# Optimization experiments

Measured on AMD Instinct MI355X. Metric: run time of the kernel, lower is better.

## Reference

```python
import jax, jax.numpy as jnp
import numpy as np

NEG_INF = -1e10
LEAK = 0.01


def gatconv(x, adj, w, a_param):
    # x: [B, Cin, N]; w: [Cin, Cout]; a_param: [2*Cout, N]; adj: [N, N]
    C = w.shape[1]
    wh = jnp.einsum('biv,io->bov', x, w)                # [B, Cout, N]
    wh1 = jnp.einsum('biv,io->bov', wh, a_param[:C])    # [B, N, N]
    wh2 = jnp.einsum('biv,io->bov', wh, a_param[C:])    # [B, N, N]
    e = jax.nn.leaky_relu(wh1 + wh2, negative_slope=LEAK)
    att = jnp.where(adj[None] > 1e-6, e, NEG_INF)
    att = jax.nn.softmax(att, axis=1)                   # softmax over source nodes (dim 1)
    h = jnp.einsum('bin,bov->bon', att, wh)             # [B, Cout, N]
    return jax.nn.elu(h)                                # GATConv concat=True -> elu


def gat_mh(x, adj, w1, a1, w2, a2):
    # head=1, support_len=1; dropout is identity in eval mode.
    h = jax.nn.elu(gatconv(x, adj, w1, a1))   # inner GAT wrapper elu
    h = jax.nn.elu(gatconv(h, adj, w2, a2))   # out_att GAT wrapper elu
    return jax.nn.elu(h)                      # GAT_MH final elu


def setup_inputs() -> dict:
    key = jax.random.key(0)
    ks = jax.random.split(key, 10)
    B, C, N, T = 8, 32, 512, 12
    inp = jax.random.normal(ks[0], (B, C, N, T), dtype=jnp.float32)
    cell = jax.random.normal(ks[1], (B, C, N, 1), dtype=jnp.float32)
    u = jax.random.uniform(ks[2], (N, N), dtype=jnp.float32)
    adj = jnp.maximum(jnp.where(u < 0.06, 1.0, 0.0), jnp.eye(N, dtype=jnp.float32))
    # 12 timesteps x 8 GAT_MH modules, each = 2 GATConvs (inner head + out_att)
    w1 = jax.random.normal(ks[3], (T, 8, C, C), dtype=jnp.float32) * 0.05
    a1 = jax.random.normal(ks[4], (T, 8, 2 * C, N), dtype=jnp.float32) * 0.05
    w2 = jax.random.normal(ks[5], (T, 8, C, C), dtype=jnp.float32) * 0.05
    a2 = jax.random.normal(ks[6], (T, 8, 2 * C, N), dtype=jnp.float32) * 0.05
    # i/f/o/c biases, each [C, N, T]
    bias = (jax.random.uniform(ks[7], (4, C, N, T), dtype=jnp.float32) - 0.5) * (2.0 / np.sqrt(N))
    return {'input': inp, 'cell': cell, 'adj': adj, 'w1': w1, 'a1': a1, 'w2': w2, 'a2': a2, 'bias': bias}


def reference(input, cell, adj, w1, a1, w2, a2, bias):
    B, C, N, T = input.shape
    c0 = cell[..., 0]                       # [B, C, N]
    xs_t = jnp.moveaxis(input, -1, 0)       # [T, B, C, N]
    bias_t = jnp.moveaxis(bias, -1, 0)      # [T, 4, C, N]

    def step(c, xs):
        x_t, w1t, a1t, w2t, a2t, bt = xs
        stacked = jnp.concatenate([
            jnp.broadcast_to(x_t[None], (4, B, C, N)),
            jnp.broadcast_to(c[None], (4, B, C, N)),
        ], axis=0)                          # [8, B, C, N]
        outs = jax.vmap(gat_mh, in_axes=(0, None, 0, 0, 0, 0))(stacked, adj, w1t, a1t, w2t, a2t)
        g = outs[:4] + bt[:, None]          # gates from x_t, plus per-gate bias
        s = outs[4:]                        # gates from cell
        i = jax.nn.sigmoid(g[0] + s[0])
        f = jax.nn.sigmoid(g[1] + s[1])
        o = jax.nn.sigmoid(g[2] + s[2])
        ct = jnp.tanh(g[3] + s[3])
        c_new = f * c + i * ct
        H = o * jnp.tanh(c_new)
        return c_new, H

    c_final, Hs = jax.lax.scan(step, c0, (xs_t, w1, a1, w2, a2, bias_t))
    output = jnp.moveaxis(Hs, 0, -1)        # [B, C, N, T]
    return output, c_final[..., None]
```

## Files before the change

### kernel.cpp

```cpp
#include <hip/hip_runtime.h>

typedef unsigned long long u64;

#define BB 8
#define CC 32
#define NN 512
#define TT 12
#define NBLK (BB*CC)

__device__ __forceinline__ float eluf(float x) {
  return x > 0.0f ? x : (expf(x) - 1.0f);
}
__device__ __forceinline__ float sigmf(float x) {
  if (x >= 0.0f) return 1.0f / (1.0f + expf(-x));
  float e = expf(x);
  return e / (1.0f + e);
}

__device__ __forceinline__ u64 pack_slot(unsigned tag, float v) {
  return ((u64)tag << 32) | (u64)__float_as_uint(v);
}

__global__ __launch_bounds__(256, 1)
void glstm_fused(const float* __restrict__ xg,
                 const float* __restrict__ cellg,
                 const float* __restrict__ w1g,
                 const float* __restrict__ w2g,
                 const float* __restrict__ biasg,
                 float* __restrict__ outg,
                 u64* slots)
{
  __shared__ float biasL[4][TT][NN];
  __shared__ float preS[4];
  __shared__ float redS[4];
  __shared__ float wpart[13][4];

  const int blk  = blockIdx.x;
  const int b    = blk >> 5;
  const int tid  = threadIdx.x;
  const int lane = tid & 63;
  const int wv   = tid >> 6;
  const int ch   = blk & 31;

  u64* csum_slot = slots;
  u64* xsum_slot = slots + 2*NBLK;

  float c0 = cellg[blk*NN + 2*tid];
  float c1 = cellg[blk*NN + 2*tid + 1];

  float xs[TT];
  #pragma unroll
  for (int t=0;t<TT;t++) xs[t]=0.0f;
  const float* xrow = xg + blk*NN*TT;
  #pragma unroll
  for (int half=0; half<2; half++){
    int n = tid + half*256;
    const float4* p = (const float4*)(xrow + n*TT);
    float4 v0=p[0], v1=p[1], v2=p[2];
    xs[0]+=v0.x;  xs[1]+=v0.y;  xs[2]+=v0.z;  xs[3]+=v0.w;
    xs[4]+=v1.x;  xs[5]+=v1.y;  xs[6]+=v1.z;  xs[7]+=v1.w;
    xs[8]+=v2.x;  xs[9]+=v2.y;  xs[10]+=v2.z; xs[11]+=v2.w;
  }
  float cpart = c0 + c1;
  #pragma unroll
  for (int off=32; off>=1; off>>=1){
    #pragma unroll
    for (int t=0;t<TT;t++) xs[t] += __shfl_xor(xs[t], off, 64);
    cpart += __shfl_xor(cpart, off, 64);
  }
  if (lane == 0){
    #pragma unroll
    for (int t=0;t<TT;t++) wpart[t][wv] = xs[t];
    wpart[12][wv] = cpart;
  }

  #pragma unroll
  for (int k=0;k<4;k++){
    #pragma unroll
    for (int half=0; half<2; half++){
      int n = tid + half*256;
      const float4* p = (const float4*)(biasg + ((k*CC + ch)*NN + n)*TT);
      float4 v0=p[0], v1=p[1], v2=p[2];
      biasL[k][0][n]=v0.x;  biasL[k][1][n]=v0.y;  biasL[k][2][n]=v0.z;  biasL[k][3][n]=v0.w;
      biasL[k][4][n]=v1.x;  biasL[k][5][n]=v1.y;  biasL[k][6][n]=v1.z;  biasL[k][7][n]=v1.w;
      biasL[k][8][n]=v2.x;  biasL[k][9][n]=v2.y;  biasL[k][10][n]=v2.z; biasL[k][11][n]=v2.w;
    }
  }
  __syncthreads();

  if (tid < 13){
    float v = wpart[tid][0] + wpart[tid][1] + wpart[tid][2] + wpart[tid][3];
    u64 pk = pack_slot(1u, v);
    if (tid < TT)
      __hip_atomic_store(&xsum_slot[tid*NBLK + blk], pk,
                         __ATOMIC_RELAXED, __HIP_MEMORY_SCOPE_AGENT);
    else
      __hip_atomic_store(&csum_slot[blk], pk,
                         __ATOMIC_RELAXED, __HIP_MEMORY_SCOPE_AGENT);
  }

  float* outrow = outg + blk*NN*TT;

  for (int s=0; s<TT; s++){
    const int i0 = lane & 31;
    u64* slot = (lane < 32)
      ? &xsum_slot[s*NBLK + b*CC + i0]
      : &csum_slot[(s&1)*NBLK + b*CC + i0];
    const unsigned want = (lane < 32) ? 1u : (unsigned)(s+1);
    u64 v = __hip_atomic_load(slot, __ATOMIC_RELAXED, __HIP_MEMORY_SCOPE_AGENT);
    int guard = 0;
    while ((unsigned)(v >> 32) != want){
      __builtin_amdgcn_s_sleep(1);
      v = __hip_atomic_load(slot, __ATOMIC_RELAXED, __HIP_MEMORY_SCOPE_AGENT);
      if (++guard > 1000000) break;
    }
    float zs = __uint_as_float((unsigned)v);

    const int m = wv + ((lane >> 5) << 2);
    const float* w1m = w1g + (s*8 + m)*CC*CC + i0;
    float s1 = 0.0f;
    #pragma unroll
    for (int j=0;j<CC;j++){
      float a = __shfl(zs, j, 32);
      s1 = fmaf(a, w1m[j*CC], s1);
    }
    float h1 = eluf(eluf(s1));
    float pp = h1 * w2g[((s*8 + m)*CC + i0)*CC + ch];
    #pragma unroll
    for (int off=16; off>=1; off>>=1) pp += __shfl_xor(pp, off, 32);
    float ov = eluf(eluf(eluf(512.0f * pp)));
    float prew = ov + __shfl_xor(ov, 32, 64);
    if (lane == 0) preS[wv] = prew;
    __syncthreads();
    const float g0 = preS[0], g1 = preS[1], g2 = preS[2], g3 = preS[3];

    const int n0 = 2*tid;
    float ig0 = sigmf(g0 + biasL[0][s][n0]);
    float fg0 = sigmf(g1 + biasL[1][s][n0]);
    float ct0 = tanhf(g3 + biasL[3][s][n0]);
    float ig1 = sigmf(g0 + biasL[0][s][n0+1]);
    float fg1 = sigmf(g1 + biasL[1][s][n0+1]);
    float ct1 = tanhf(g3 + biasL[3][s][n0+1]);
    c0 = fg0*c0 + ig0*ct0;
    c1 = fg1*c1 + ig1*ct1;
    float csp = c0 + c1;
    __syncthreads();

    if (s < TT-1){
      #pragma unroll
      for (int off=32; off>=1; off>>=1) csp += __shfl_xor(csp, off, 64);
      if (lane == 0) redS[wv] = csp;
      __syncthreads();
      if (tid == 0){
        float tot = redS[0]+redS[1]+redS[2]+redS[3];
        __hip_atomic_store(&csum_slot[((s+1)&1)*NBLK + blk],
                           pack_slot((unsigned)(s+2), tot),
                           __ATOMIC_RELAXED, __HIP_MEMORY_SCOPE_AGENT);
      }
    }

    float og0 = sigmf(g2 + biasL[2][s][n0]);
    float og1 = sigmf(g2 + biasL[2][s][n0+1]);
    outrow[n0*TT + s]     = og0 * tanhf(c0);
    outrow[(n0+1)*TT + s] = og1 * tanhf(c1);
  }

  float* cf = outg + NBLK*NN*TT + blk*NN;
  cf[2*tid]   = c0;
  cf[2*tid+1] = c1;
}

extern "C" void kernel_launch(void* const* d_in, const int* in_sizes, int n_in,
                              void* d_out, int out_size, void* d_ws, size_t ws_size,
                              hipStream_t stream)
{
  (void)in_sizes; (void)n_in; (void)out_size; (void)ws_size;
  const float* xg    = (const float*)d_in[0];
  const float* cellg = (const float*)d_in[1];
  const float* w1g   = (const float*)d_in[3];
  const float* w2g   = (const float*)d_in[5];
  const float* biasg = (const float*)d_in[7];
  float* outg = (float*)d_out;
  u64* slots = (u64*)d_ws;

  hipMemsetAsync(d_ws, 0, (size_t)(2*NBLK + TT*NBLK)*sizeof(u64), stream);
  glstm_fused<<<dim3(NBLK), dim3(256), 0, stream>>>(xg, cellg, w1g, w2g, biasg, outg, slots);
}
```

Measured before the change: 48.92 us.

## Precompute x-path gates before recurrence and shorten per-step cross-block sync

```diff
diff --git a/kernel.cpp b/kernel.cpp
--- a/kernel.cpp
+++ b/kernel.cpp
@@ -2,26 +2,28 @@
 
 typedef unsigned long long u64;
 
-#define BB 8
 #define CC 32
 #define NN 512
 #define TT 12
-#define NBLK (BB*CC)
-
-__device__ __forceinline__ float eluf(float x) {
-  return x > 0.0f ? x : (expf(x) - 1.0f);
-}
-__device__ __forceinline__ float sigmf(float x) {
-  if (x >= 0.0f) return 1.0f / (1.0f + expf(-x));
-  float e = expf(x);
-  return e / (1.0f + e);
-}
-
-__device__ __forceinline__ u64 pack_slot(unsigned tag, float v) {
-  return ((u64)tag << 32) | (u64)__float_as_uint(v);
-}
-
-__global__ __launch_bounds__(256, 1)
+#define NBLK 256
+#define NTHR 512
+
+__device__ __forceinline__ float eluf(float x){ return x>0.f ? x : (expf(x)-1.f); }
+__device__ __forceinline__ float sigmf(float x){
+  if (x>=0.f) return 1.f/(1.f+expf(-x));
+  float e=expf(x); return e/(1.f+e);
+}
+__device__ __forceinline__ u64 pack_slot(unsigned tag, float v){
+  return ((u64)tag<<32) | (u64)__float_as_uint(v);
+}
+__device__ __forceinline__ u64 ld_slot(u64* p){
+  return __hip_atomic_load(p, __ATOMIC_RELAXED, __HIP_MEMORY_SCOPE_AGENT);
+}
+__device__ __forceinline__ void st_slot(u64* p, u64 v){
+  __hip_atomic_store(p, v, __ATOMIC_RELAXED, __HIP_MEMORY_SCOPE_AGENT);
+}
+
+__global__ __launch_bounds__(NTHR, 1)
 void glstm_fused(const float* __restrict__ xg,
                  const float* __restrict__ cellg,
                  const float* __restrict__ w1g,
@@ -30,144 +32,158 @@
                  float* __restrict__ outg,
                  u64* slots)
 {
-  __shared__ float biasL[4][TT][NN];
-  __shared__ float preS[4];
-  __shared__ float redS[4];
-  __shared__ float wpart[13][4];
+  __shared__ float preS[2][4];
+  __shared__ float xpart[TT][8];
 
   const int blk  = blockIdx.x;
-  const int b    = blk >> 5;
+  const int b    = blk & 7;
+  const int ch   = blk >> 3;
+  const int row  = b*CC + ch;
   const int tid  = threadIdx.x;
   const int lane = tid & 63;
   const int wv   = tid >> 6;
-  const int ch   = blk & 31;
-
-  u64* csum_slot = slots;
-  u64* xsum_slot = slots + 2*NBLK;
-
-  float c0 = cellg[blk*NN + 2*tid];
-  float c1 = cellg[blk*NN + 2*tid + 1];
+  const int i0   = lane & 31;
+  const int jbase = (lane >> 5) << 4;
+  const int pbase = (lane >> 5) << 2;
+
+  u64* csum_part = slots;
+  u64* xsum_slot = slots + 2*8*NBLK;
+
+  const int n0 = tid;
+  float c = cellg[row*NN + n0];
+
+  float bias0[TT], bias1[TT], bias2[TT], bias3[TT];
+  #pragma unroll
+  for (int k=0;k<4;k++){
+    const float4* p = (const float4*)(biasg + ((k*CC+ch)*NN + n0)*TT);
+    float4 v0=p[0], v1=p[1], v2=p[2];
+    float* dst = (k==0)?bias0:(k==1)?bias1:(k==2)?bias2:bias3;
+    dst[0]=v0.x; dst[1]=v0.y; dst[2]=v0.z;  dst[3]=v0.w;
+    dst[4]=v1.x; dst[5]=v1.y; dst[6]=v1.z;  dst[7]=v1.w;
+    dst[8]=v2.x; dst[9]=v2.y; dst[10]=v2.z; dst[11]=v2.w;
+  }
 
   float xs[TT];
-  #pragma unroll
-  for (int t=0;t<TT;t++) xs[t]=0.0f;
-  const float* xrow = xg + blk*NN*TT;
-  #pragma unroll
-  for (int half=0; half<2; half++){
-    int n = tid + half*256;
-    const float4* p = (const float4*)(xrow + n*TT);
+  {
+    const float4* p = (const float4*)(xg + (row*NN + n0)*TT);
     float4 v0=p[0], v1=p[1], v2=p[2];
-    xs[0]+=v0.x;  xs[1]+=v0.y;  xs[2]+=v0.z;  xs[3]+=v0.w;
-    xs[4]+=v1.x;  xs[5]+=v1.y;  xs[6]+=v1.z;  xs[7]+=v1.w;
-    xs[8]+=v2.x;  xs[9]+=v2.y;  xs[10]+=v2.z; xs[11]+=v2.w;
-  }
-  float cpart = c0 + c1;
+    xs[0]=v0.x; xs[1]=v0.y; xs[2]=v0.z;  xs[3]=v0.w;
+    xs[4]=v1.x; xs[5]=v1.y; xs[6]=v1.z;  xs[7]=v1.w;
+    xs[8]=v2.x; xs[9]=v2.y; xs[10]=v2.z; xs[11]=v2.w;
+  }
+  float cp = c;
   #pragma unroll
   for (int off=32; off>=1; off>>=1){
     #pragma unroll
     for (int t=0;t<TT;t++) xs[t] += __shfl_xor(xs[t], off, 64);
-    cpart += __shfl_xor(cpart, off, 64);
-  }
-  if (lane == 0){
-    #pragma unroll
-    for (int t=0;t<TT;t++) wpart[t][wv] = xs[t];
-    wpart[12][wv] = cpart;
-  }
-
+    cp += __shfl_xor(cp, off, 64);
+  }
+  if (lane==0){
+    #pragma unroll
+    for (int t=0;t<TT;t++) xpart[t][wv] = xs[t];
+    st_slot(&csum_part[wv*NBLK + row], pack_slot(1u, cp));
+  }
+  __syncthreads();
+  if (tid < TT){
+    float v = 0.f;
+    #pragma unroll
+    for (int w8=0; w8<8; w8++) v += xpart[tid][w8];
+    st_slot(&xsum_slot[tid*NBLK + row], pack_slot(1u, v));
+  }
+
+  float ovx[TT];
+  if (wv < 4){
+    const int m = wv;
+    #pragma unroll
+    for (int s=0;s<TT;s++){
+      u64* sl = &xsum_slot[s*NBLK + b*CC + i0];
+      u64 v = ld_slot(sl);
+      int guard = 0;
+      while ((unsigned)(v>>32) != 1u){
+        __builtin_amdgcn_s_sleep(1);
+        v = ld_slot(sl);
+        if (++guard > 1000000) break;
+      }
+      float zs = __uint_as_float((unsigned)v);
+      const float* w1m = w1g + (s*8+m)*CC*CC + i0;
+      float part = 0.f;
+      #pragma unroll
+      for (int jj=0;jj<16;jj++){
+        int j = jbase + jj;
+        float a = __shfl(zs, j, 32);
+        part = fmaf(a, w1m[j*CC], part);
+      }
+      float s1 = part + __shfl_xor(part, 32, 64);
+      float h1 = eluf(eluf(s1));
+      float pp = h1 * w2g[((s*8+m)*CC + i0)*CC + ch];
+      #pragma unroll
+      for (int off=16; off>=1; off>>=1) pp += __shfl_xor(pp, off, 32);
+      ovx[s] = eluf(eluf(eluf(512.f*pp)));
+    }
+  }
+
+  float hm[TT];
   #pragma unroll
-  for (int k=0;k<4;k++){
-    #pragma unroll
-    for (int half=0; half<2; half++){
-      int n = tid + half*256;
-      const float4* p = (const float4*)(biasg + ((k*CC + ch)*NN + n)*TT);
-      float4 v0=p[0], v1=p[1], v2=p[2];
-      biasL[k][0][n]=v0.x;  biasL[k][1][n]=v0.y;  biasL[k][2][n]=v0.z;  biasL[k][3][n]=v0.w;
-      biasL[k][4][n]=v1.x;  biasL[k][5][n]=v1.y;  biasL[k][6][n]=v1.z;  biasL[k][7][n]=v1.w;
-      biasL[k][8][n]=v2.x;  biasL[k][9][n]=v2.y;  biasL[k][10][n]=v2.z; biasL[k][11][n]=v2.w;
+  for (int s=0;s<TT;s++){
+    if (wv < 4){
+      const int m = wv + 4;
+      const unsigned want = (unsigned)(s+1);
+      u64* base = &csum_part[(((s&1)<<3) + pbase)*NBLK + b*CC + i0];
+      u64 v0,v1,v2,v3; int guard = 0;
+      for(;;){
+        v0 = ld_slot(base);
+        v1 = ld_slot(base +   NBLK);
+        v2 = ld_slot(base + 2*NBLK);
+        v3 = ld_slot(base + 3*NBLK);
+        if ((unsigned)(v0>>32)==want && (unsigned)(v1>>32)==want &&
+            (unsigned)(v2>>32)==want && (unsigned)(v3>>32)==want) break;
+        __builtin_amdgcn_s_sleep(1);
+        if (++guard > 1000000) break;
+      }
+      float zh = __uint_as_float((unsigned)v0) + __uint_as_float((unsigned)v1)
+               + __uint_as_float((unsigned)v2) + __uint_as_float((unsigned)v3);
+      float zs = zh + __shfl_xor(zh, 32, 64);
+      const float* w1m = w1g + (s*8+m)*CC*CC + i0;
+      float part = 0.f;
+      #pragma unroll
+      for (int jj=0;jj<16;jj++){
+        int j = jbase + jj;
+        float a = __shfl(zs, j, 32);
+        part = fmaf(a, w1m[j*CC], part);
+      }
+      float s1 = part + __shfl_xor(part, 32, 64);
+      float h1 = eluf(eluf(s1));
+      float pp = h1 * w2g[((s*8+m)*CC + i0)*CC + ch];
+      #pragma unroll
+      for (int off=16; off>=1; off>>=1) pp += __shfl_xor(pp, off, 32);
+      float ovc = eluf(eluf(eluf(512.f*pp)));
+      if (lane==0) preS[s&1][wv] = ovx[s] + ovc;
     }
-  }
-  __syncthreads();
-
-  if (tid < 13){
-    float v = wpart[tid][0] + wpart[tid][1] + wpart[tid][2] + wpart[tid][3];
-    u64 pk = pack_slot(1u, v);
-    if (tid < TT)
-      __hip_atomic_store(&xsum_slot[tid*NBLK + blk], pk,
-                         __ATOMIC_RELAXED, __HIP_MEMORY_SCOPE_AGENT);
-    else
-      __hip_atomic_store(&csum_slot[blk], pk,
-                         __ATOMIC_RELAXED, __HIP_MEMORY_SCOPE_AGENT);
-  }
-
-  float* outrow = outg + blk*NN*TT;
-
-  for (int s=0; s<TT; s++){
-    const int i0 = lane & 31;
-    u64* slot = (lane < 32)
-      ? &xsum_slot[s*NBLK + b*CC + i0]
-      : &csum_slot[(s&1)*NBLK + b*CC + i0];
-    const unsigned want = (lane < 32) ? 1u : (unsigned)(s+1);
-    u64 v = __hip_atomic_load(slot, __ATOMIC_RELAXED, __HIP_MEMORY_SCOPE_AGENT);
-    int guard = 0;
-    while ((unsigned)(v >> 32) != want){
-      __builtin_amdgcn_s_sleep(1);
-      v = __hip_atomic_load(slot, __ATOMIC_RELAXED, __HIP_MEMORY_SCOPE_AGENT);
-      if (++guard > 1000000) break;
+    __syncthreads();
+    const float g0 = preS[s&1][0], g1 = preS[s&1][1];
+    const float g2 = preS[s&1][2], g3 = preS[s&1][3];
+
+    float ig = sigmf(g0 + bias0[s]);
+    float fg = sigmf(g1 + bias1[s]);
+    float ct = tanhf(g3 + bias3[s]);
+    c = fg*c + ig*ct;
+
+    if (s < TT-1){
+      float csp = c;
+      #pragma unroll
+      for (int off=32; off>=1; off>>=1) csp += __shfl_xor(csp, off, 64);
+      if (lane==0)
+        st_slot(&csum_part[((((s+1)&1)<<3) + wv)*NBLK + row],
+                pack_slot((unsigned)(s+2), csp));
     }
-    float zs = __uint_as_float((unsigned)v);
-
-    const int m = wv + ((lane >> 5) << 2);
-    const float* w1m = w1g + (s*8 + m)*CC*CC + i0;
-    float s1 = 0.0f;
-    #pragma unroll
-    for (int j=0;j<CC;j++){
-      float a = __shfl(zs, j, 32);
-      s1 = fmaf(a, w1m[j*CC], s1);
-    }
-    float h1 = eluf(eluf(s1));
-    float pp = h1 * w2g[((s*8 + m)*CC + i0)*CC + ch];
-    #pragma unroll
-    for (int off=16; off>=1; off>>=1) pp += __shfl_xor(pp, off, 32);
-    float ov = eluf(eluf(eluf(512.0f * pp)));
-    float prew = ov + __shfl_xor(ov, 32, 64);
-    if (lane == 0) preS[wv] = prew;
-    __syncthreads();
-    const float g0 = preS[0], g1 = preS[1], g2 = preS[2], g3 = preS[3];
-
-    const int n0 = 2*tid;
-    float ig0 = sigmf(g0 + biasL[0][s][n0]);
-    float fg0 = sigmf(g1 + biasL[1][s][n0]);
-    float ct0 = tanhf(g3 + biasL[3][s][n0]);
-    float ig1 = sigmf(g0 + biasL[0][s][n0+1]);
-    float fg1 = sigmf(g1 + biasL[1][s][n0+1]);
-    float ct1 = tanhf(g3 + biasL[3][s][n0+1]);
-    c0 = fg0*c0 + ig0*ct0;
-    c1 = fg1*c1 + ig1*ct1;
-    float csp = c0 + c1;
-    __syncthreads();
-
-    if (s < TT-1){
-      #pragma unroll
-      for (int off=32; off>=1; off>>=1) csp += __shfl_xor(csp, off, 64);
-      if (lane == 0) redS[wv] = csp;
-      __syncthreads();
-      if (tid == 0){
-        float tot = redS[0]+redS[1]+redS[2]+redS[3];
-        __hip_atomic_store(&csum_slot[((s+1)&1)*NBLK + blk],
-                           pack_slot((unsigned)(s+2), tot),
-                           __ATOMIC_RELAXED, __HIP_MEMORY_SCOPE_AGENT);
-      }
-    }
-
-    float og0 = sigmf(g2 + biasL[2][s][n0]);
-    float og1 = sigmf(g2 + biasL[2][s][n0+1]);
-    outrow[n0*TT + s]     = og0 * tanhf(c0);
-    outrow[(n0+1)*TT + s] = og1 * tanhf(c1);
-  }
-
-  float* cf = outg + NBLK*NN*TT + blk*NN;
-  cf[2*tid]   = c0;
-  cf[2*tid+1] = c1;
+    hm[s] = sigmf(g2 + bias2[s]) * tanhf(c);
+  }
+
+  float4* op = (float4*)(outg + (row*NN + n0)*TT);
+  op[0] = make_float4(hm[0], hm[1], hm[2],  hm[3]);
+  op[1] = make_float4(hm[4], hm[5], hm[6],  hm[7]);
+  op[2] = make_float4(hm[8], hm[9], hm[10], hm[11]);
+  outg[NBLK*NN*TT + row*NN + n0] = c;
 }
 
 extern "C" void kernel_launch(void* const* d_in, const int* in_sizes, int n_in,
@@ -183,6 +199,6 @@
   float* outg = (float*)d_out;
   u64* slots = (u64*)d_ws;
 
-  hipMemsetAsync(d_ws, 0, (size_t)(2*NBLK + TT*NBLK)*sizeof(u64), stream);
-  glstm_fused<<<dim3(NBLK), dim3(256), 0, stream>>>(xg, cellg, w1g, w2g, biasg, outg, slots);
-}
+  hipMemsetAsync(d_ws, 0, (size_t)(2*8*NBLK + TT*NBLK)*sizeof(u64), stream);
+  glstm_fused<<<dim3(NBLK), dim3(NTHR), 0, stream>>>(xg, cellg, w1g, w2g, biasg, outg, slots);
+}
```

Measured after the change: 111.3 us. +127.5%, slower.
